# Kernel optimization log

Measured on AMD Instinct MI355X. Metric: run time of the kernel, lower is better.

Reference implementation:

```python
import jax, jax.numpy as jnp
import numpy as np

SEQ, PREV, BS, D_IN, H, D = 512, 512, 8, 1024, 16, 64


def setup_inputs() -> dict:
    key = jax.random.key(0)
    ks = jax.random.split(key, 10)
    s = 0.02
    inp = {
        "input_": jax.random.normal(ks[0], (SEQ, BS, D_IN), jnp.float32),
        "pos_embs": jax.random.normal(ks[1], (SEQ + PREV, D_IN), jnp.float32),
        "memory": jax.random.normal(ks[2], (PREV, BS, D_IN), jnp.float32),
        "u": jax.random.normal(ks[3], (H, D), jnp.float32) * s,
        "v": jax.random.normal(ks[4], (H, D), jnp.float32) * s,
        # causal mask allowing full attention to memory: triu with diagonal=1+prev
        "mask": (jnp.triu(jnp.ones((SEQ, SEQ + PREV), jnp.bool_), k=1 + PREV))[..., None],
        "W_kv": jax.random.normal(ks[5], (D_IN, 2 * H * D), jnp.float32) * s,
        "W_q": jax.random.normal(ks[6], (D_IN, H * D), jnp.float32) * s,
        "W_p": jax.random.normal(ks[7], (D_IN, H * D), jnp.float32) * s,
        "W_out": jax.random.normal(ks[8], (H * D, D_IN), jnp.float32) * s,
        "ln_gamma": jnp.ones((D_IN,), jnp.float32),
        "ln_beta": jnp.zeros((D_IN,), jnp.float32),
    }
    return inp


def _rel_shift(x):
    # x: (q, k, bs, H) -> pad one zero column, reshape-transpose trick, drop first row
    q, k, bs, h = x.shape
    zp = jnp.zeros((q, 1, bs, h), x.dtype)
    return jnp.concatenate([zp, x], axis=1).reshape(k + 1, q, bs, h)[1:].reshape(q, k, bs, h)


def reference(input_, pos_embs, memory, u, v, mask, W_kv, W_q, W_p, W_out, ln_gamma, ln_beta):
    cur_seq, bs, d_in = input_.shape
    prev_seq = memory.shape[0]
    tot = cur_seq + prev_seq
    h, d = u.shape
    scale = 1.0 / d ** 0.5

    iwm = jnp.concatenate([memory, input_], axis=0)          # (tot, bs, d_in)
    kv = jnp.einsum('jbe,ef->jbf', iwm, W_kv)                 # (tot, bs, 2*H*d)
    k_t, v_t = jnp.split(kv, 2, axis=-1)
    q_t = jnp.einsum('ibe,ef->ibf', input_, W_q)              # (cur, bs, H*d)

    q4 = q_t.reshape(cur_seq, bs, h, d)
    k4 = k_t.reshape(tot, bs, h, d)
    v4 = v_t.reshape(tot, bs, h, d)

    content_attn = jnp.einsum('ibhd,jbhd->ijbh', q4 + u, k4)  # (cur, tot, bs, H)

    p_t = (pos_embs @ W_p).reshape(tot, h, d)                 # (tot, H, d)
    position_attn = jnp.einsum('ibhd,jhd->ijbh', q4 + v, p_t)
    position_attn = _rel_shift(position_attn)

    attn = content_attn + position_attn
    attn = jnp.where(mask[..., None], -jnp.inf, attn)         # mask: (cur, tot, 1) -> (cur, tot, 1, 1)
    attn = jax.nn.softmax(attn * scale, axis=1)

    awv = jnp.einsum('ijbh,jbhd->ibhd', attn, v4).reshape(cur_seq, bs, h * d)
    out = input_ + awv @ W_out                                # residual

    mu = jnp.mean(out, axis=-1, keepdims=True)
    var = jnp.mean((out - mu) ** 2, axis=-1, keepdims=True)
    out = (out - mu) / jnp.sqrt(var + 1e-5) * ln_gamma + ln_beta
    return out
```

## Files before the change

kernel.cpp:

```cpp
#include <hip/hip_runtime.h>
#include <math.h>

#define SEQ  512
#define PREV 512
#define TOT  1024
#define BSZ  8
#define DIN  1024
#define NH   16
#define HD   64

typedef __bf16 bf16;
typedef __bf16 bf16x8 __attribute__((ext_vector_type(8)));
typedef float  f32x4  __attribute__((ext_vector_type(4)));
typedef float  f32x16 __attribute__((ext_vector_type(16)));
typedef unsigned int u32;
typedef u32 u32x2 __attribute__((ext_vector_type(2)));

__device__ __forceinline__ f32x4 MFMA16(bf16x8 a, bf16x8 b, f32x4 c) {
    return __builtin_amdgcn_mfma_f32_16x16x32_bf16(a, b, c, 0, 0, 0);
}
__device__ __forceinline__ f32x16 MFMA32(bf16x8 a, bf16x8 b, f32x16 c) {
    return __builtin_amdgcn_mfma_f32_32x32x16_bf16(a, b, c, 0, 0, 0);
}

#define GLOAD16(g, l) __builtin_amdgcn_global_load_lds( \
    (const __attribute__((address_space(1))) void*)(g), \
    (__attribute__((address_space(3))) void*)(l), 16, 0, 0)

__device__ __forceinline__ unsigned short bfbits(float x) {
    return __builtin_bit_cast(unsigned short, (bf16)x);
}
__device__ __forceinline__ float bf2f(u32 bits16) {
    return __builtin_bit_cast(float, bits16 << 16);
}

__global__ __launch_bounds__(256) void prep_all(
    const float* __restrict__ memory, const float* __restrict__ input_,
    const float* __restrict__ pos,
    const float* __restrict__ W_kv, const float* __restrict__ W_q,
    const float* __restrict__ W_p,  const float* __restrict__ W_out,
    bf16* __restrict__ iwm, bf16* __restrict__ posb,
    bf16* __restrict__ wkv, bf16* __restrict__ wq,
    bf16* __restrict__ wp,  bf16* __restrict__ wo)
{
    __shared__ float tile[32][33];
    const int bid = blockIdx.x;
    const int t = threadIdx.x;
    if (bid < 9216) {
        const float* src; bf16* dst; int e4;
        if (bid < 8192) {
            e4 = (bid * 256 + t) * 4;
            src = (e4 < 4194304) ? memory : input_ - 4194304;
            dst = iwm;
        } else {
            e4 = ((bid - 8192) * 256 + t) * 4;
            src = pos; dst = posb;
        }
        float4 x = *(const float4*)(src + e4);
        union { bf16 h[4]; ushort4 u4; } pk;
        pk.h[0] = (bf16)x.x; pk.h[1] = (bf16)x.y; pk.h[2] = (bf16)x.z; pk.h[3] = (bf16)x.w;
        *(ushort4*)(dst + e4) = pk.u4;
        return;
    }
    const int rem = bid - 9216;
    const int bx = rem % 160, by = rem / 160;
    const float* W; bf16* Wt; int N, bn;
    if (bx < 64)       { W = W_kv;  Wt = wkv; N = 2048; bn = bx * 32; }
    else if (bx < 96)  { W = W_q;   Wt = wq;  N = 1024; bn = (bx - 64) * 32; }
    else if (bx < 128) { W = W_p;   Wt = wp;  N = 1024; bn = (bx - 96) * 32; }
    else               { W = W_out; Wt = wo;  N = 1024; bn = (bx - 128) * 32; }
    const int bk = by * 32;
    const int r = t >> 3, c4 = (t & 7) * 4;
    float4 x = *(const float4*)(W + (size_t)(bk + r) * N + bn + c4);
    tile[r][c4 + 0] = x.x; tile[r][c4 + 1] = x.y;
    tile[r][c4 + 2] = x.z; tile[r][c4 + 3] = x.w;
    __syncthreads();
    union { bf16 h[4]; ushort4 u4; } pk;
#pragma unroll
    for (int i = 0; i < 4; ++i) pk.h[i] = (bf16)tile[c4 + i][r];
    *(ushort4*)(Wt + (size_t)(bn + r) * 1024 + bk + c4) = pk.u4;
}

__global__ __launch_bounds__(512, 1) void gemm_8ph(
    const bf16* __restrict__ A, const bf16* __restrict__ Bt,
    bf16* __restrict__ C, int M, int N, int K)
{
    __shared__ __align__(16) bf16 A_s[2][256 * 64];
    __shared__ __align__(16) bf16 B_s[2][256 * 64];
    const int t = threadIdx.x;
    const int w = t >> 6, lane = t & 63;
    const int li = lane & 15, hi = lane >> 4;
    const int wm = w >> 2, wn = w & 3;
    const int lin = blockIdx.y * 8 + blockIdx.x;
    const int xcd = lin & 7, idx = lin >> 3;
    const int bm = (xcd * 4 + (idx & 3)) * 256;
    const int bn = (idx >> 2) * 256;

    f32x4 acc[8][4];
#pragma unroll
    for (int m = 0; m < 8; ++m)
#pragma unroll
        for (int n = 0; n < 4; ++n) acc[m][n] = (f32x4){0.f, 0.f, 0.f, 0.f};

    auto stage_half = [&](int buf, int ks, int h) {
        const bf16* __restrict__ src = (h < 2) ? A : Bt;
        const int base = (h < 2) ? bm : bn;
        const int hh = (h & 1) * 128;
        bf16* dst = (h < 2) ? &A_s[buf][0] : &B_s[buf][0];
        const int k0 = ks << 6;
#pragma unroll
        for (int g = 0; g < 2; ++g) {
            const int row = hh + g * 64 + (t >> 3);
            const bf16* gp = src + (size_t)(base + row) * K + k0 + (((t & 7) ^ (row & 7)) * 8);
            GLOAD16(gp, dst + (size_t)(hh + g * 64 + w * 8) * 64);
        }
    };

    bf16x8 af[4], bfr[4];
    auto LDA = [&](int buf, int mh, int kk) {
#pragma unroll
        for (int m = 0; m < 4; ++m) {
            int row = wm * 128 + (mh * 4 + m) * 16 + li;
            af[m] = *(const bf16x8*)&A_s[buf][row * 64 + (((kk * 4 + hi) ^ (row & 7)) * 8)];
        }
    };
    auto LDB = [&](int buf, int kk) {
#pragma unroll
        for (int n = 0; n < 4; ++n) {
            int row = wn * 64 + n * 16 + li;
            bfr[n] = *(const bf16x8*)&B_s[buf][row * 64 + (((kk * 4 + hi) ^ (row & 7)) * 8)];
        }
    };

#define FMA_PHASE(mh)                                                    \
    asm volatile("s_waitcnt lgkmcnt(0)" ::: "memory");                   \
    __builtin_amdgcn_sched_barrier(0);                                   \
    __builtin_amdgcn_s_setprio(1);                                       \
    _Pragma("unroll")                                                    \
    for (int m = 0; m < 4; ++m)                                          \
        _Pragma("unroll")                                                \
        for (int n = 0; n < 4; ++n)                                      \
            acc[(mh) * 4 + m][n] = MFMA16(af[m], bfr[n], acc[(mh) * 4 + m][n]); \
    __builtin_amdgcn_s_setprio(0);

    stage_half(0, 0, 0); stage_half(0, 0, 1); stage_half(0, 0, 2); stage_half(0, 0, 3);

    const int nk = K >> 6;
    for (int ks = 0; ks < nk; ++ks) {
        const int cur = ks & 1, nxt = cur ^ 1;
        asm volatile("s_waitcnt vmcnt(0)" ::: "memory");
        __builtin_amdgcn_sched_barrier(0);
        __builtin_amdgcn_s_barrier();
        __builtin_amdgcn_sched_barrier(0);
        if (ks + 1 < nk) {
            stage_half(nxt, ks + 1, 0); stage_half(nxt, ks + 1, 1);
            stage_half(nxt, ks + 1, 2); stage_half(nxt, ks + 1, 3);
        }
        LDB(cur, 0); LDA(cur, 0, 0);
        FMA_PHASE(0)
        LDA(cur, 1, 0);
        FMA_PHASE(1)
        LDB(cur, 1); LDA(cur, 0, 1);
        FMA_PHASE(0)
        LDA(cur, 1, 1);
        FMA_PHASE(1)
    }

#pragma unroll
    for (int m = 0; m < 8; ++m)
#pragma unroll
        for (int n = 0; n < 4; ++n)
#pragma unroll
            for (int r = 0; r < 4; ++r) {
                int row = bm + wm * 128 + m * 16 + hi * 4 + r;
                int col = bn + wn * 64 + n * 16 + li;
                C[(size_t)row * N + col] = (bf16)acc[m][n][r];
            }
#undef FMA_PHASE
}

__global__ __launch_bounds__(256) void gemm_out(
    const bf16* __restrict__ A, const bf16* __restrict__ Bt,
    const float* __restrict__ Rres, float* __restrict__ Cf, int N, int K)
{
    __shared__ __align__(16) bf16 A_s[128 * 64];
    __shared__ __align__(16) bf16 B_s[128 * 64];
    const int t = threadIdx.x;
    const int w = t >> 6, lane = t & 63;
    const int li = lane & 15, hi = lane >> 4;
    const int wr = w >> 1, wc = w & 1;
    const int bm = blockIdx.y * 128, bn = blockIdx.x * 128;
    const int l3 = lane >> 3, l7 = lane & 7;
    const int srcoct = ((l7 ^ l3) * 8);

    f32x4 acc[4][4];
#pragma unroll
    for (int m = 0; m < 4; ++m)
#pragma unroll
        for (int n = 0; n < 4; ++n) acc[m][n] = (f32x4){0.f, 0.f, 0.f, 0.f};

    auto stage = [&](int k0) {
#pragma unroll
        for (int i = 0; i < 4; ++i) {
            int c = w * 4 + i;
            GLOAD16(A + (size_t)(bm + c * 8 + l3) * K + k0 + srcoct, &A_s[c * 512]);
            GLOAD16(Bt + (size_t)(bn + c * 8 + l3) * K + k0 + srcoct, &B_s[c * 512]);
        }
    };

    stage(0);
    const int nk = K >> 6;
    for (int ks = 0; ks < nk; ++ks) {
        __syncthreads();
#pragma unroll
        for (int kk = 0; kk < 2; ++kk) {
            bf16x8 af[4], bfr[4];
#pragma unroll
            for (int m = 0; m < 4; ++m) {
                int row = wr * 64 + m * 16 + li;
                af[m] = *(const bf16x8*)&A_s[row * 64 + ((kk * 32 + hi * 8) ^ ((row & 7) * 8))];
            }
#pragma unroll
            for (int n = 0; n < 4; ++n) {
                int row = wc * 64 + n * 16 + li;
                bfr[n] = *(const bf16x8*)&B_s[row * 64 + ((kk * 32 + hi * 8) ^ ((row & 7) * 8))];
            }
#pragma unroll
            for (int m = 0; m < 4; ++m)
#pragma unroll
                for (int n = 0; n < 4; ++n)
                    acc[m][n] = MFMA16(af[m], bfr[n], acc[m][n]);
        }
        __syncthreads();
        if (ks + 1 < nk) stage((ks + 1) << 6);
    }

#pragma unroll
    for (int m = 0; m < 4; ++m)
#pragma unroll
        for (int n = 0; n < 4; ++n)
#pragma unroll
            for (int r = 0; r < 4; ++r) {
                int row = bm + wr * 64 + m * 16 + hi * 4 + r;
                int col = bn + wc * 64 + n * 16 + li;
                size_t off = (size_t)row * N + col;
                Cf[off] = acc[m][n][r] + Rres[off];
            }
}

__global__ __launch_bounds__(256) void gemm_qp(
    const bf16* __restrict__ iwmq, const bf16* __restrict__ posb,
    const bf16* __restrict__ wq, const bf16* __restrict__ wp,
    bf16* __restrict__ qbf, bf16* __restrict__ pbf)
{
    __shared__ __align__(16) bf16 A_s[128 * 64];
    __shared__ __align__(16) bf16 B_s[128 * 64];
    const int t = threadIdx.x;
    const int w = t >> 6, lane = t & 63;
    const int li = lane & 15, hi = lane >> 4;
    const int wr = w >> 1, wc = w & 1;
    const int by = blockIdx.y;
    const bf16* A; const bf16* Bt; bf16* Cb; int bm;
    if (by < 32) { A = iwmq; Bt = wq; Cb = qbf; bm = by * 128; }
    else         { A = posb; Bt = wp; Cb = pbf; bm = (by - 32) * 128; }
    const int bn = blockIdx.x * 128;
    const int l3 = lane >> 3, l7 = lane & 7;
    const int srcoct = ((l7 ^ l3) * 8);

    f32x4 acc[4][4];
#pragma unroll
    for (int m = 0; m < 4; ++m)
#pragma unroll
        for (int n = 0; n < 4; ++n) acc[m][n] = (f32x4){0.f, 0.f, 0.f, 0.f};

    auto stage = [&](int k0) {
#pragma unroll
        for (int i = 0; i < 4; ++i) {
            int c = w * 4 + i;
            GLOAD16(A + (size_t)(bm + c * 8 + l3) * 1024 + k0 + srcoct, &A_s[c * 512]);
            GLOAD16(Bt + (size_t)(bn + c * 8 + l3) * 1024 + k0 + srcoct, &B_s[c * 512]);
        }
    };

    stage(0);
    for (int ks = 0; ks < 16; ++ks) {
        __syncthreads();
#pragma unroll
        for (int kk = 0; kk < 2; ++kk) {
            bf16x8 af[4], bfr[4];
#pragma unroll
            for (int m = 0; m < 4; ++m) {
                int row = wr * 64 + m * 16 + li;
                af[m] = *(const bf16x8*)&A_s[row * 64 + ((kk * 32 + hi * 8) ^ ((row & 7) * 8))];
            }
#pragma unroll
            for (int n = 0; n < 4; ++n) {
                int row = wc * 64 + n * 16 + li;
                bfr[n] = *(const bf16x8*)&B_s[row * 64 + ((kk * 32 + hi * 8) ^ ((row & 7) * 8))];
            }
#pragma unroll
            for (int m = 0; m < 4; ++m)
#pragma unroll
                for (int n = 0; n < 4; ++n)
                    acc[m][n] = MFMA16(af[m], bfr[n], acc[m][n]);
        }
        __syncthreads();
        if (ks + 1 < 16) stage((ks + 1) << 6);
    }

#pragma unroll
    for (int m = 0; m < 4; ++m)
#pragma unroll
        for (int n = 0; n < 4; ++n)
#pragma unroll
            for (int r = 0; r < 4; ++r) {
                int row = bm + wr * 64 + m * 16 + hi * 4 + r;
                int col = bn + wc * 64 + n * 16 + li;
                Cb[(size_t)row * 1024 + col] = (bf16)acc[m][n][r];
            }
}

__global__ __launch_bounds__(256, 2) void attn_mfma(
    const bf16* __restrict__ kv, const bf16* __restrict__ qb,
    const bf16* __restrict__ pb, const float* __restrict__ u,
    const float* __restrict__ v, bf16* __restrict__ awv)
{
    const int bi = (blockIdx.z & 1) ? (3 - blockIdx.x) : blockIdx.x;
    const int i0 = bi * 128;
    const int b  = blockIdx.y;
    const int h  = blockIdx.z;
    const int t  = threadIdx.x;
    const int w  = t >> 6;
    const int lane = t & 63;
    const int ql  = lane & 31;
    const int hi2 = lane >> 5;

    __shared__ __align__(16) bf16 K_s[64 * 64];
    __shared__ __align__(16) bf16 V_s[64][72];
    __shared__ __align__(16) bf16 P_s[256 * 64];
    __shared__ __align__(16) char SCR[4][6912];

    char* rsc = SCR[w];

    const int c8 = t & 7;
    const int rq = t >> 3;
    const int nt = 2 * bi + 10;
    const int C0 = 384 - i0;

    bf16x8 vreg[2];
#pragma unroll
    for (int p = 0; p < 2; ++p)
        vreg[p] = *(const bf16x8*)(kv + (size_t)((p * 32 + rq) * BSZ + b) * 2048 + 1024 + h * HD + c8 * 8);
#pragma unroll
    for (int p = 0; p < 2; ++p)
        GLOAD16(kv + (size_t)((p * 32 + rq) * BSZ + b) * 2048 + h * HD + ((c8 ^ (rq & 7)) * 8),
                K_s + (p * 32 + rq) * 64 + c8 * 8);
#pragma unroll
    for (int cp = 0; cp < 6; ++cp) {
        int grow = C0 + cp * 32 + rq;
        GLOAD16(pb + (size_t)grow * DIN + h * HD + ((c8 ^ (rq & 7)) * 8),
                P_s + (grow & 255) * 64 + c8 * 8);
    }

    bf16x8 qu[4], qv[4];
    {
        const size_t qoff = ((size_t)(i0 + w * 32 + ql) * BSZ + b) * DIN + h * HD;
#pragma unroll
        for (int kk = 0; kk < 4; ++kk) {
            bf16x8 q8 = *(const bf16x8*)(qb + qoff + kk * 16 + hi2 * 8);
            const float* up = u + h * HD + kk * 16 + hi2 * 8;
            const float* vp = v + h * HD + kk * 16 + hi2 * 8;
#pragma unroll
            for (int m = 0; m < 8; ++m) {
                float qf = (float)q8[m];
                qu[kk][m] = (bf16)(qf + up[m]);
                qv[kk][m] = (bf16)(qf + vp[m]);
            }
        }
    }

    float mrun = -1e30f, lrun = 0.f;
    f32x16 o[2];
    o[0] = (f32x16){}; o[1] = (f32x16){};

    const int phq = (31 - ql) & 3;
    const int sel = phq >> 1;
    const int shb = (phq & 1) * 16;

    for (int tt = 0; tt < nt; ++tt) {
        const int j0 = tt * 64;

        __builtin_amdgcn_s_barrier();
        __builtin_amdgcn_sched_barrier(0);

#pragma unroll
        for (int p = 0; p < 2; ++p) {
            int j = p * 32 + rq;
#pragma unroll
            for (int mm = 0; mm < 8; ++mm)
                V_s[c8 * 8 + mm][(j + 8 * c8) & 63] = vreg[p][mm];
        }
        asm volatile("s_waitcnt vmcnt(0) lgkmcnt(0)" ::: "memory");
        __builtin_amdgcn_sched_barrier(0);
        __builtin_amdgcn_s_barrier();
        __builtin_amdgcn_sched_barrier(0);

        f32x16 st[2];
        st[0] = (f32x16){}; st[1] = (f32x16){};
        __builtin_amdgcn_s_setprio(1);
#pragma unroll
        for (int jt = 0; jt < 2; ++jt) {
            int row = jt * 32 + ql;
#pragma unroll
            for (int kk = 0; kk < 4; ++kk) {
                bf16x8 kf = *(const bf16x8*)&K_s[row * 64 + (((kk * 2 + hi2) ^ (ql & 7)) * 8)];
                st[jt] = MFMA32(kf, qu[kk], st[jt]);
            }
        }
        const int bwg = j0 - i0 + 480 - 32 * w;
        f32x16 rp[3];
        rp[0] = (f32x16){}; rp[1] = (f32x16){}; rp[2] = (f32x16){};
#pragma unroll
        for (int Rt = 0; Rt < 3; ++Rt) {
            int ring = (bwg + Rt * 32 + ql) & 255;
#pragma unroll
            for (int kk = 0; kk < 4; ++kk) {
                bf16x8 pf = *(const bf16x8*)&P_s[ring * 64 + (((kk * 2 + hi2) ^ (ring & 7)) * 8)];
                rp[Rt] = MFMA32(pf, qv[kk], rp[Rt]);
            }
        }
        __builtin_amdgcn_s_setprio(0);

#pragma unroll
        for (int Rt = 0; Rt < 3; ++Rt)
#pragma unroll
            for (int a = 0; a < 4; ++a) {
                u32 lo = (u32)bfbits(rp[Rt][a * 4 + 0]) | ((u32)bfbits(rp[Rt][a * 4 + 1]) << 16);
                u32 hi = (u32)bfbits(rp[Rt][a * 4 + 2]) | ((u32)bfbits(rp[Rt][a * 4 + 3]) << 16);
                *(u32x2*)(rsc + ql * 216 + 64 * Rt + 16 * a + 8 * hi2) = (u32x2){lo, hi};
            }

        __builtin_amdgcn_s_barrier();
        __builtin_amdgcn_sched_barrier(0);

        if (tt + 1 < nt) {
            const int j0n = j0 + 64;
#pragma unroll
            for (int p = 0; p < 2; ++p)
                vreg[p] = *(const bf16x8*)(kv + (size_t)((j0n + p * 32 + rq) * BSZ + b) * 2048 + 1024 + h * HD + c8 * 8);
#pragma unroll
            for (int p = 0; p < 2; ++p)
                GLOAD16(kv + (size_t)((j0n + p * 32 + rq) * BSZ + b) * 2048 + h * HD + ((c8 ^ (rq & 7)) * 8),
                        K_s + (p * 32 + rq) * 64 + c8 * 8);
        }
        if (tt + 3 < nt) {
            const int Cs = C0 + (tt + 3) * 64;
#pragma unroll
            for (int p = 0; p < 2; ++p) {
                int grow = Cs + p * 32 + rq;
                GLOAD16(pb + (size_t)grow * DIN + h * HD + ((c8 ^ (rq & 7)) * 8),
                        P_s + (grow & 255) * 64 + c8 * 8);
            }
        }

        float rowmax = -1e30f;
        const int limb = i0 + 32 * w + ql + PREV - j0;
        auto assemble = [&](bool domask) {
#pragma unroll
            for (int jt = 0; jt < 2; ++jt)
#pragma unroll
                for (int a = 0; a < 4; ++a) {
                    int e = jt * 32 + 8 * a + 4 * hi2 + 31 - ql;
                    const u32x2* W = (const u32x2*)(rsc + ql * 216 + 8 * (e >> 2));
                    u32x2 A0 = W[0], A1 = W[1];
                    u32 U0 = sel ? A0[1] : A0[0];
                    u32 U1 = sel ? A1[0] : A0[1];
                    u32 U2 = sel ? A1[1] : A1[0];
                    u32 o0 = (u32)((((unsigned long long)U1 << 32) | U0) >> shb);
                    u32 o1 = (u32)((((unsigned long long)U2 << 32) | U1) >> shb);
                    float pq[4] = {bf2f(o0 & 0xffffu), bf2f(o0 >> 16),
                                   bf2f(o1 & 0xffffu), bf2f(o1 >> 16)};
#pragma unroll
                    for (int rr = 0; rr < 4; ++rr) {
                        int r = a * 4 + rr;
                        int lj = jt * 32 + 8 * a + 4 * hi2 + rr;
                        float sv = (st[jt][r] + pq[rr]) * 0.125f;
                        if (domask && lj > limb) sv = -1e30f;
                        st[jt][r] = sv;
                        rowmax = fmaxf(rowmax, sv);
                    }
                }
        };
        if (__builtin_amdgcn_readfirstlane(j0 + 63 - (i0 + 32 * w + PREV)) > 0)
            assemble(true);
        else
            assemble(false);

        {
            u32 rm = __builtin_bit_cast(u32, rowmax), rm2 = rm;
            asm("v_permlane32_swap_b32 %0, %1" : "+v"(rm), "+v"(rm2));
            rowmax = fmaxf(__builtin_bit_cast(float, rm2), __builtin_bit_cast(float, rm) * 0.f + rowmax);
            rowmax = fmaxf(rowmax, __builtin_bit_cast(float, rm2));
        }

        if (!__all(rowmax - mrun <= 8.f)) {
            float newm = fmaxf(mrun, rowmax);
            float fsc = __expf(mrun - newm);
#pragma unroll
            for (int r = 0; r < 16; ++r) {
                float fr = __shfl(fsc, (r & 3) + 8 * (r >> 2) + 4 * hi2);
                o[0][r] *= fr; o[1][r] *= fr;
            }
            lrun *= fsc;
            mrun = newm;
        }
        float rowsum = 0.f;
#pragma unroll
        for (int jt = 0; jt < 2; ++jt)
#pragma unroll
            for (int r = 0; r < 16; ++r) {
                float p = __expf(st[jt][r] - mrun);
                st[jt][r] = p;
                rowsum += p;
            }
        {
            u32 rs = __builtin_bit_cast(u32, rowsum), rs2 = rs;
            asm("v_permlane32_swap_b32 %0, %1" : "+v"(rs), "+v"(rs2));
            rowsum += __builtin_bit_cast(float, rs2);
        }
        lrun += rowsum;

        u32 pk0[2][4], pk1[2][4];
#pragma unroll
        for (int jt = 0; jt < 2; ++jt)
#pragma unroll
            for (int a = 0; a < 4; ++a) {
                pk0[jt][a] = (u32)bfbits(st[jt][a * 4 + 0]) | ((u32)bfbits(st[jt][a * 4 + 1]) << 16);
                pk1[jt][a] = (u32)bfbits(st[jt][a * 4 + 2]) | ((u32)bfbits(st[jt][a * 4 + 3]) << 16);
            }

        __builtin_amdgcn_s_setprio(1);
#pragma unroll
        for (int js = 0; js < 4; ++js) {
            const int jt = js >> 1, a0 = 2 * (js & 1), a1 = a0 + 1;
            u32 w0 = pk0[jt][a0], w2 = pk0[jt][a1];
            asm("v_permlane32_swap_b32 %0, %1" : "+v"(w0), "+v"(w2));
            u32 w1 = pk1[jt][a0], w3 = pk1[jt][a1];
            asm("v_permlane32_swap_b32 %0, %1" : "+v"(w1), "+v"(w3));
            union { u32 uw[4]; bf16x8 vv; } pa;
            pa.uw[0] = w0; pa.uw[1] = w1; pa.uw[2] = w2; pa.uw[3] = w3;
#pragma unroll
            for (int dt = 0; dt < 2; ++dt) {
                int dcol = dt * 32 + ql;
                int colb = (js * 16 + hi2 * 8 + 8 * (dcol >> 3)) & 63;
                bf16x8 vf = *(const bf16x8*)&V_s[dcol][colb];
                o[dt] = MFMA32(pa.vv, vf, o[dt]);
            }
        }
        __builtin_amdgcn_s_setprio(0);
    }

    float linv = __builtin_amdgcn_rcpf(lrun);
    float lr[16];
#pragma unroll
    for (int r = 0; r < 16; ++r) lr[r] = __shfl(linv, (r & 3) + 8 * (r >> 2) + 4 * hi2);
#pragma unroll
    for (int dt = 0; dt < 2; ++dt)
#pragma unroll
        for (int r = 0; r < 16; ++r) {
            int row = i0 + 32 * w + (r & 3) + 8 * (r >> 2) + 4 * hi2;
            awv[((size_t)row * BSZ + b) * DIN + h * HD + dt * 32 + ql] = (bf16)(o[dt][r] * lr[r]);
        }
}

__global__ __launch_bounds__(256) void ln_f32(
    float* __restrict__ out, const float* __restrict__ gamma, const float* __restrict__ beta)
{
    const int row = blockIdx.x;
    const int t = threadIdx.x;
    float4 x = *(float4*)(out + (size_t)row * DIN + t * 4);
    float s  = x.x + x.y + x.z + x.w;
    float ss = x.x * x.x + x.y * x.y + x.z * x.z + x.w * x.w;
#pragma unroll
    for (int wd = 1; wd < 64; wd <<= 1) { s += __shfl_xor(s, wd); ss += __shfl_xor(ss, wd); }
    __shared__ float sbuf[4], ssbuf[4];
    const int wave = t >> 6, lanei = t & 63;
    if (lanei == 0) { sbuf[wave] = s; ssbuf[wave] = ss; }
    __syncthreads();
    s  = sbuf[0] + sbuf[1] + sbuf[2] + sbuf[3];
    ss = ssbuf[0] + ssbuf[1] + ssbuf[2] + ssbuf[3];
    const float mu   = s * (1.f / DIN);
    const float var  = ss * (1.f / DIN) - mu * mu;
    const float rstd = rsqrtf(var + 1e-5f);
    float4 g  = *(const float4*)(gamma + t * 4);
    float4 bb = *(const float4*)(beta + t * 4);
    float4 y;
    y.x = (x.x - mu) * rstd * g.x + bb.x;
    y.y = (x.y - mu) * rstd * g.y + bb.y;
    y.z = (x.z - mu) * rstd * g.z + bb.z;
    y.w = (x.w - mu) * rstd * g.w + bb.w;
    *(float4*)(out + (size_t)row * DIN + t * 4) = y;
}

extern "C" void kernel_launch(void* const* d_in, const int* in_sizes, int n_in,
                              void* d_out, int out_size, void* d_ws, size_t ws_size,
                              hipStream_t stream)
{
    const float* input_ = (const float*)d_in[0];
    const float* pos    = (const float*)d_in[1];
    const float* memory = (const float*)d_in[2];
    const float* u      = (const float*)d_in[3];
    const float* v      = (const float*)d_in[4];
    const float* W_kv   = (const float*)d_in[6];
    const float* W_q    = (const float*)d_in[7];
    const float* W_p    = (const float*)d_in[8];
    const float* W_out  = (const float*)d_in[9];
    const float* gamma  = (const float*)d_in[10];
    const float* beta   = (const float*)d_in[11];

    bf16* iwm  = (bf16*)d_ws;
    bf16* kvb  = iwm  + (size_t)8192 * 1024;
    bf16* qbf  = kvb  + (size_t)8192 * 2048;
    bf16* pbf  = qbf  + (size_t)4096 * 1024;
    bf16* posb = pbf  + (size_t)1024 * 1024;
    bf16* wkv  = posb + (size_t)1024 * 1024;
    bf16* wq   = wkv  + (size_t)2048 * 1024;
    bf16* wp   = wq   + (size_t)1024 * 1024;
    bf16* wo   = wp   + (size_t)1024 * 1024;
    bf16* awvb = wo   + (size_t)1024 * 1024;
    float* outf = (float*)d_out;

    prep_all<<<14336, 256, 0, stream>>>(memory, input_, pos, W_kv, W_q, W_p, W_out,
                                        iwm, posb, wkv, wq, wp, wo);

    gemm_8ph<<<dim3(8, 32), 512, 0, stream>>>(iwm, wkv, kvb, 8192, 2048, 1024);
    gemm_qp<<<dim3(8, 40), 256, 0, stream>>>(iwm + (size_t)4096 * 1024, posb, wq, wp, qbf, pbf);

    attn_mfma<<<dim3(4, 8, 16), 256, 0, stream>>>(kvb, qbf, pbf, u, v, awvb);

    gemm_out<<<dim3(8, 32), 256, 0, stream>>>(awvb, wo, input_, outf, 1024, 1024);
    ln_f32<<<4096, 256, 0, stream>>>(outf, gamma, beta);
}
```

Before: 170.4 us.

## Switch KV GEMM to 32x32 MFMA with 4 waves and double-buffer output GEMM

The KV projection GEMM moves from 8 waves using 16x16x32 MFMAs to 4 waves using 32x32x16 MFMAs, each wave owning a 128x128 sub-tile. Staging and LDS reads are rewritten for the new fragment layout. The output GEMM gains double-buffered LDS with loads prefetched one step ahead, a single barrier per step, and raised wave priority around its MFMAs. A rowmax reduction in attention is also simplified. The larger MFMA shape aims for more compute per LDS read, at the cost of fewer waves to hide latency and higher register pressure.

```diff
diff --git a/kernel.cpp b/kernel.cpp
--- a/kernel.cpp
+++ b/kernel.cpp
@@ -81,7 +81,7 @@
     *(ushort4*)(Wt + (size_t)(bn + r) * 1024 + bk + c4) = pk.u4;
 }
 
-__global__ __launch_bounds__(512, 1) void gemm_8ph(
+__global__ __launch_bounds__(256, 1) void gemm_kv(
     const bf16* __restrict__ A, const bf16* __restrict__ Bt,
     bf16* __restrict__ C, int M, int N, int K)
 {
@@ -89,18 +89,20 @@
     __shared__ __align__(16) bf16 B_s[2][256 * 64];
     const int t = threadIdx.x;
     const int w = t >> 6, lane = t & 63;
-    const int li = lane & 15, hi = lane >> 4;
-    const int wm = w >> 2, wn = w & 3;
+    const int ql = lane & 31, hi2 = lane >> 5;
+    const int wm = w >> 1, wn = w & 1;
     const int lin = blockIdx.y * 8 + blockIdx.x;
     const int xcd = lin & 7, idx = lin >> 3;
     const int bm = (xcd * 4 + (idx & 3)) * 256;
     const int bn = (idx >> 2) * 256;
 
-    f32x4 acc[8][4];
-#pragma unroll
-    for (int m = 0; m < 8; ++m)
-#pragma unroll
-        for (int n = 0; n < 4; ++n) acc[m][n] = (f32x4){0.f, 0.f, 0.f, 0.f};
+    f32x16 acc[4][4];
+#pragma unroll
+    for (int mf = 0; mf < 4; ++mf)
+#pragma unroll
+        for (int nf = 0; nf < 4; ++nf) acc[mf][nf] = (f32x16){};
+
+    const int l7 = lane & 7, l3 = lane >> 3;
 
     auto stage_half = [&](int buf, int ks, int h) {
         const bf16* __restrict__ src = (h < 2) ? A : Bt;
@@ -109,39 +111,28 @@
         bf16* dst = (h < 2) ? &A_s[buf][0] : &B_s[buf][0];
         const int k0 = ks << 6;
 #pragma unroll
-        for (int g = 0; g < 2; ++g) {
-            const int row = hh + g * 64 + (t >> 3);
-            const bf16* gp = src + (size_t)(base + row) * K + k0 + (((t & 7) ^ (row & 7)) * 8);
-            GLOAD16(gp, dst + (size_t)(hh + g * 64 + w * 8) * 64);
+        for (int g = 0; g < 4; ++g) {
+            const int row = hh + g * 32 + 8 * w + l3;
+            const bf16* gp = src + (size_t)(base + row) * K + k0 + ((l7 ^ (row & 7)) * 8);
+            GLOAD16(gp, dst + (size_t)row * 64 + l7 * 8);
         }
     };
 
     bf16x8 af[4], bfr[4];
-    auto LDA = [&](int buf, int mh, int kk) {
-#pragma unroll
-        for (int m = 0; m < 4; ++m) {
-            int row = wm * 128 + (mh * 4 + m) * 16 + li;
-            af[m] = *(const bf16x8*)&A_s[buf][row * 64 + (((kk * 4 + hi) ^ (row & 7)) * 8)];
+    auto LDA = [&](int buf, int kt) {
+#pragma unroll
+        for (int mf = 0; mf < 4; ++mf) {
+            int row = wm * 128 + mf * 32 + ql;
+            af[mf] = *(const bf16x8*)&A_s[buf][(size_t)row * 64 + (((kt * 2 + hi2) ^ (row & 7)) * 8)];
         }
     };
-    auto LDB = [&](int buf, int kk) {
-#pragma unroll
-        for (int n = 0; n < 4; ++n) {
-            int row = wn * 64 + n * 16 + li;
-            bfr[n] = *(const bf16x8*)&B_s[buf][row * 64 + (((kk * 4 + hi) ^ (row & 7)) * 8)];
+    auto LDB = [&](int buf, int kt) {
+#pragma unroll
+        for (int nf = 0; nf < 4; ++nf) {
+            int row = wn * 128 + nf * 32 + ql;
+            bfr[nf] = *(const bf16x8*)&B_s[buf][(size_t)row * 64 + (((kt * 2 + hi2) ^ (row & 7)) * 8)];
         }
     };
-
-#define FMA_PHASE(mh)                                                    \
-    asm volatile("s_waitcnt lgkmcnt(0)" ::: "memory");                   \
-    __builtin_amdgcn_sched_barrier(0);                                   \
-    __builtin_amdgcn_s_setprio(1);                                       \
-    _Pragma("unroll")                                                    \
-    for (int m = 0; m < 4; ++m)                                          \
-        _Pragma("unroll")                                                \
-        for (int n = 0; n < 4; ++n)                                      \
-            acc[(mh) * 4 + m][n] = MFMA16(af[m], bfr[n], acc[(mh) * 4 + m][n]); \
-    __builtin_amdgcn_s_setprio(0);
 
     stage_half(0, 0, 0); stage_half(0, 0, 1); stage_half(0, 0, 2); stage_half(0, 0, 3);
 
@@ -156,35 +147,39 @@
             stage_half(nxt, ks + 1, 0); stage_half(nxt, ks + 1, 1);
             stage_half(nxt, ks + 1, 2); stage_half(nxt, ks + 1, 3);
         }
-        LDB(cur, 0); LDA(cur, 0, 0);
-        FMA_PHASE(0)
-        LDA(cur, 1, 0);
-        FMA_PHASE(1)
-        LDB(cur, 1); LDA(cur, 0, 1);
-        FMA_PHASE(0)
-        LDA(cur, 1, 1);
-        FMA_PHASE(1)
+#pragma unroll
+        for (int kt = 0; kt < 4; ++kt) {
+            LDA(cur, kt); LDB(cur, kt);
+            asm volatile("s_waitcnt lgkmcnt(0)" ::: "memory");
+            __builtin_amdgcn_sched_barrier(0);
+            __builtin_amdgcn_s_setprio(1);
+#pragma unroll
+            for (int mf = 0; mf < 4; ++mf)
+#pragma unroll
+                for (int nf = 0; nf < 4; ++nf)
+                    acc[mf][nf] = MFMA32(af[mf], bfr[nf], acc[mf][nf]);
+            __builtin_amdgcn_s_setprio(0);
+        }
     }
 
 #pragma unroll
-    for (int m = 0; m < 8; ++m)
-#pragma unroll
-        for (int n = 0; n < 4; ++n)
-#pragma unroll
-            for (int r = 0; r < 4; ++r) {
-                int row = bm + wm * 128 + m * 16 + hi * 4 + r;
-                int col = bn + wn * 64 + n * 16 + li;
-                C[(size_t)row * N + col] = (bf16)acc[m][n][r];
-            }
-#undef FMA_PHASE
+    for (int mf = 0; mf < 4; ++mf)
+#pragma unroll
+        for (int nf = 0; nf < 4; ++nf)
+#pragma unroll
+            for (int r = 0; r < 16; ++r) {
+                int row = bm + wm * 128 + mf * 32 + (r & 3) + 8 * (r >> 2) + 4 * hi2;
+                int col = bn + wn * 128 + nf * 32 + ql;
+                C[(size_t)row * N + col] = (bf16)acc[mf][nf][r];
+            }
 }
 
 __global__ __launch_bounds__(256) void gemm_out(
     const bf16* __restrict__ A, const bf16* __restrict__ Bt,
     const float* __restrict__ Rres, float* __restrict__ Cf, int N, int K)
 {
-    __shared__ __align__(16) bf16 A_s[128 * 64];
-    __shared__ __align__(16) bf16 B_s[128 * 64];
+    __shared__ __align__(16) bf16 A_s[2][128 * 64];
+    __shared__ __align__(16) bf16 B_s[2][128 * 64];
     const int t = threadIdx.x;
     const int w = t >> 6, lane = t & 63;
     const int li = lane & 15, hi = lane >> 4;
@@ -199,40 +194,47 @@
 #pragma unroll
         for (int n = 0; n < 4; ++n) acc[m][n] = (f32x4){0.f, 0.f, 0.f, 0.f};
 
-    auto stage = [&](int k0) {
+    auto stage = [&](int buf, int k0) {
 #pragma unroll
         for (int i = 0; i < 4; ++i) {
             int c = w * 4 + i;
-            GLOAD16(A + (size_t)(bm + c * 8 + l3) * K + k0 + srcoct, &A_s[c * 512]);
-            GLOAD16(Bt + (size_t)(bn + c * 8 + l3) * K + k0 + srcoct, &B_s[c * 512]);
+            GLOAD16(A + (size_t)(bm + c * 8 + l3) * K + k0 + srcoct, &A_s[buf][c * 512]);
+            GLOAD16(Bt + (size_t)(bn + c * 8 + l3) * K + k0 + srcoct, &B_s[buf][c * 512]);
         }
     };
 
-    stage(0);
+    stage(0, 0);
     const int nk = K >> 6;
     for (int ks = 0; ks < nk; ++ks) {
-        __syncthreads();
+        const int cur = ks & 1, nxt = cur ^ 1;
+        asm volatile("s_waitcnt vmcnt(0)" ::: "memory");
+        __builtin_amdgcn_sched_barrier(0);
+        __builtin_amdgcn_s_barrier();
+        __builtin_amdgcn_sched_barrier(0);
+        if (ks + 1 < nk) stage(nxt, (ks + 1) << 6);
 #pragma unroll
         for (int kk = 0; kk < 2; ++kk) {
             bf16x8 af[4], bfr[4];
 #pragma unroll
             for (int m = 0; m < 4; ++m) {
                 int row = wr * 64 + m * 16 + li;
-                af[m] = *(const bf16x8*)&A_s[row * 64 + ((kk * 32 + hi * 8) ^ ((row & 7) * 8))];
+                af[m] = *(const bf16x8*)&A_s[cur][row * 64 + ((kk * 32 + hi * 8) ^ ((row & 7) * 8))];
             }
 #pragma unroll
             for (int n = 0; n < 4; ++n) {
                 int row = wc * 64 + n * 16 + li;
-                bfr[n] = *(const bf16x8*)&B_s[row * 64 + ((kk * 32 + hi * 8) ^ ((row & 7) * 8))];
-            }
+                bfr[n] = *(const bf16x8*)&B_s[cur][row * 64 + ((kk * 32 + hi * 8) ^ ((row & 7) * 8))];
+            }
+            asm volatile("s_waitcnt lgkmcnt(0)" ::: "memory");
+            __builtin_amdgcn_sched_barrier(0);
+            __builtin_amdgcn_s_setprio(1);
 #pragma unroll
             for (int m = 0; m < 4; ++m)
 #pragma unroll
                 for (int n = 0; n < 4; ++n)
                     acc[m][n] = MFMA16(af[m], bfr[n], acc[m][n]);
-        }
-        __syncthreads();
-        if (ks + 1 < nk) stage((ks + 1) << 6);
+            __builtin_amdgcn_s_setprio(0);
+        }
     }
 
 #pragma unroll
@@ -499,7 +501,7 @@
         {
             u32 rm = __builtin_bit_cast(u32, rowmax), rm2 = rm;
             asm("v_permlane32_swap_b32 %0, %1" : "+v"(rm), "+v"(rm2));
-            rowmax = fmaxf(__builtin_bit_cast(float, rm2), __builtin_bit_cast(float, rm) * 0.f + rowmax);
+            rowmax = fmaxf(rowmax, __builtin_bit_cast(float, rm));
             rowmax = fmaxf(rowmax, __builtin_bit_cast(float, rm2));
         }
 
@@ -633,7 +635,7 @@
     prep_all<<<14336, 256, 0, stream>>>(memory, input_, pos, W_kv, W_q, W_p, W_out,
                                         iwm, posb, wkv, wq, wp, wo);
 
-    gemm_8ph<<<dim3(8, 32), 512, 0, stream>>>(iwm, wkv, kvb, 8192, 2048, 1024);
+    gemm_kv<<<dim3(8, 32), 256, 0, stream>>>(iwm, wkv, kvb, 8192, 2048, 1024);
     gemm_qp<<<dim3(8, 40), 256, 0, stream>>>(iwm + (size_t)4096 * 1024, posb, wq, wp, qbf, pbf);
 
     attn_mfma<<<dim3(4, 8, 16), 256, 0, stream>>>(kvb, qbf, pbf, u, v, awvb);
```

Measured after the change: 174.0 us. 1.02x slower.

## Fuse fp32-to-bf16 activation conversion into GEMMs, double-buffer gemm_out, use exp2 softmax

Applied to the files above, without the earlier changes.

Stops pre-converting memory, input and pos_embs to bf16 in a separate pass. The KV and Q/P GEMMs now load the fp32 rows directly, convert them in registers and write swizzled bf16 into LDS, which removes a full write and re-read of the activations. gemm_out gets double-buffered LDS with explicit waitcnt and priority hints. The attention softmax folds log2(e) into the scale and uses a raw v_exp_f32, with the rescale threshold adjusted to match. The cost is more VGPR pressure and extra conversion work inside the GEMM loops, and the fp32 A loads are now regular register loads rather than direct-to-LDS.

```diff
diff --git a/kernel.cpp b/kernel.cpp
--- a/kernel.cpp
+++ b/kernel.cpp
@@ -33,43 +33,27 @@
 __device__ __forceinline__ float bf2f(u32 bits16) {
     return __builtin_bit_cast(float, bits16 << 16);
 }
-
-__global__ __launch_bounds__(256) void prep_all(
-    const float* __restrict__ memory, const float* __restrict__ input_,
-    const float* __restrict__ pos,
+__device__ __forceinline__ float exp2_raw(float x) {
+    float r;
+    asm("v_exp_f32 %0, %1" : "=v"(r) : "v"(x));
+    return r;
+}
+
+__global__ __launch_bounds__(256) void prep_w(
     const float* __restrict__ W_kv, const float* __restrict__ W_q,
     const float* __restrict__ W_p,  const float* __restrict__ W_out,
-    bf16* __restrict__ iwm, bf16* __restrict__ posb,
     bf16* __restrict__ wkv, bf16* __restrict__ wq,
     bf16* __restrict__ wp,  bf16* __restrict__ wo)
 {
     __shared__ float tile[32][33];
-    const int bid = blockIdx.x;
+    const int bx = blockIdx.x;
     const int t = threadIdx.x;
-    if (bid < 9216) {
-        const float* src; bf16* dst; int e4;
-        if (bid < 8192) {
-            e4 = (bid * 256 + t) * 4;
-            src = (e4 < 4194304) ? memory : input_ - 4194304;
-            dst = iwm;
-        } else {
-            e4 = ((bid - 8192) * 256 + t) * 4;
-            src = pos; dst = posb;
-        }
-        float4 x = *(const float4*)(src + e4);
-        union { bf16 h[4]; ushort4 u4; } pk;
-        pk.h[0] = (bf16)x.x; pk.h[1] = (bf16)x.y; pk.h[2] = (bf16)x.z; pk.h[3] = (bf16)x.w;
-        *(ushort4*)(dst + e4) = pk.u4;
-        return;
-    }
-    const int rem = bid - 9216;
-    const int bx = rem % 160, by = rem / 160;
     const float* W; bf16* Wt; int N, bn;
     if (bx < 64)       { W = W_kv;  Wt = wkv; N = 2048; bn = bx * 32; }
     else if (bx < 96)  { W = W_q;   Wt = wq;  N = 1024; bn = (bx - 64) * 32; }
     else if (bx < 128) { W = W_p;   Wt = wp;  N = 1024; bn = (bx - 96) * 32; }
     else               { W = W_out; Wt = wo;  N = 1024; bn = (bx - 128) * 32; }
-    const int bk = by * 32;
+    const int bk = blockIdx.y * 32;
     const int r = t >> 3, c4 = (t & 7) * 4;
     float4 x = *(const float4*)(W + (size_t)(bk + r) * N + bn + c4);
     tile[r][c4 + 0] = x.x; tile[r][c4 + 1] = x.y;
@@ -81,9 +65,9 @@
     *(ushort4*)(Wt + (size_t)(bn + r) * 1024 + bk + c4) = pk.u4;
 }
 
-__global__ __launch_bounds__(512, 1) void gemm_8ph(
-    const bf16* __restrict__ A, const bf16* __restrict__ Bt,
-    bf16* __restrict__ C, int M, int N, int K)
+__global__ __launch_bounds__(512, 1) void gemm_kv(
+    const float* __restrict__ memory, const float* __restrict__ input_,
+    const bf16* __restrict__ wkv, bf16* __restrict__ kvb)
 {
     __shared__ __align__(16) bf16 A_s[2][256 * 64];
     __shared__ __align__(16) bf16 B_s[2][256 * 64];
@@ -95,6 +79,9 @@
     const int xcd = lin & 7, idx = lin >> 3;
     const int bm = (xcd * 4 + (idx & 3)) * 256;
     const int bn = (idx >> 2) * 256;
+    const float* __restrict__ srcA = (bm < 4096) ? memory + (size_t)bm * 1024
+                                                 : input_ + (size_t)(bm - 4096) * 1024;
+    const int arow = t >> 1, aoct = (t & 1) * 4;
 
     f32x4 acc[8][4];
 #pragma unroll
@@ -102,17 +89,33 @@
 #pragma unroll
         for (int n = 0; n < 4; ++n) acc[m][n] = (f32x4){0.f, 0.f, 0.f, 0.f};
 
-    auto stage_half = [&](int buf, int ks, int h) {
-        const bf16* __restrict__ src = (h < 2) ? A : Bt;
-        const int base = (h < 2) ? bm : bn;
-        const int hh = (h & 1) * 128;
-        bf16* dst = (h < 2) ? &A_s[buf][0] : &B_s[buf][0];
+    float4 areg[4][2];
+    auto issueA = [&](int ks) {
+        const float* rp = srcA + (size_t)arow * 1024 + ks * 64;
+#pragma unroll
+        for (int c = 0; c < 4; ++c) {
+            areg[c][0] = *(const float4*)(rp + (aoct + c) * 8);
+            areg[c][1] = *(const float4*)(rp + (aoct + c) * 8 + 4);
+        }
+    };
+    auto writeA = [&](int buf) {
+#pragma unroll
+        for (int c = 0; c < 4; ++c) {
+            union { bf16 h[8]; bf16x8 v; } pk;
+            pk.h[0] = (bf16)areg[c][0].x; pk.h[1] = (bf16)areg[c][0].y;
+            pk.h[2] = (bf16)areg[c][0].z; pk.h[3] = (bf16)areg[c][0].w;
+            pk.h[4] = (bf16)areg[c][1].x; pk.h[5] = (bf16)areg[c][1].y;
+            pk.h[6] = (bf16)areg[c][1].z; pk.h[7] = (bf16)areg[c][1].w;
+            *(bf16x8*)&A_s[buf][arow * 64 + (((aoct + c) ^ (arow & 7)) * 8)] = pk.v;
+        }
+    };
+    auto stageB = [&](int buf, int ks) {
         const int k0 = ks << 6;
 #pragma unroll
-        for (int g = 0; g < 2; ++g) {
-            const int row = hh + g * 64 + (t >> 3);
-            const bf16* gp = src + (size_t)(base + row) * K + k0 + (((t & 7) ^ (row & 7)) * 8);
-            GLOAD16(gp, dst + (size_t)(hh + g * 64 + w * 8) * 64);
+        for (int g = 0; g < 4; ++g) {
+            const int row = g * 64 + (t >> 3);
+            GLOAD16(wkv + (size_t)(bn + row) * 1024 + k0 + (((t & 7) ^ (row & 7)) * 8),
+                    &B_s[buf][(size_t)row * 64 + (t & 7) * 8]);
         }
     };
 
@@ -143,19 +146,18 @@
             acc[(mh) * 4 + m][n] = MFMA16(af[m], bfr[n], acc[(mh) * 4 + m][n]); \
     __builtin_amdgcn_s_setprio(0);
 
-    stage_half(0, 0, 0); stage_half(0, 0, 1); stage_half(0, 0, 2); stage_half(0, 0, 3);
-
-    const int nk = K >> 6;
+    issueA(0);
+    stageB(0, 0);
+    writeA(0);
+    asm volatile("s_waitcnt vmcnt(0) lgkmcnt(0)" ::: "memory");
+    __builtin_amdgcn_sched_barrier(0);
+    __builtin_amdgcn_s_barrier();
+    __builtin_amdgcn_sched_barrier(0);
+
+    const int nk = 16;
     for (int ks = 0; ks < nk; ++ks) {
         const int cur = ks & 1, nxt = cur ^ 1;
-        asm volatile("s_waitcnt vmcnt(0)" ::: "memory");
-        __builtin_amdgcn_sched_barrier(0);
-        __builtin_amdgcn_s_barrier();
-        __builtin_amdgcn_sched_barrier(0);
-        if (ks + 1 < nk) {
-            stage_half(nxt, ks + 1, 0); stage_half(nxt, ks + 1, 1);
-            stage_half(nxt, ks + 1, 2); stage_half(nxt, ks + 1, 3);
-        }
+        if (ks + 1 < nk) { issueA(ks + 1); stageB(nxt, ks + 1); }
         LDB(cur, 0); LDA(cur, 0, 0);
         FMA_PHASE(0)
         LDA(cur, 1, 0);
@@ -164,7 +166,17 @@
         FMA_PHASE(0)
         LDA(cur, 1, 1);
         FMA_PHASE(1)
+        if (ks + 1 < nk) {
+            asm volatile("s_waitcnt vmcnt(4)" ::: "memory");
+            __builtin_amdgcn_sched_barrier(0);
+            writeA(nxt);
+            asm volatile("s_waitcnt vmcnt(0) lgkmcnt(0)" ::: "memory");
+            __builtin_amdgcn_sched_barrier(0);
+        }
+        __builtin_amdgcn_s_barrier();
+        __builtin_amdgcn_sched_barrier(0);
     }
+#undef FMA_PHASE
 
 #pragma unroll
     for (int m = 0; m < 8; ++m)
@@ -174,82 +186,12 @@
             for (int r = 0; r < 4; ++r) {
                 int row = bm + wm * 128 + m * 16 + hi * 4 + r;
                 int col = bn + wn * 64 + n * 16 + li;
-                C[(size_t)row * N + col] = (bf16)acc[m][n][r];
-            }
-#undef FMA_PHASE
-}
-
-__global__ __launch_bounds__(256) void gemm_out(
-    const bf16* __restrict__ A, const bf16* __restrict__ Bt,
-    const float* __restrict__ Rres, float* __restrict__ Cf, int N, int K)
-{
-    __shared__ __align__(16) bf16 A_s[128 * 64];
-    __shared__ __align__(16) bf16 B_s[128 * 64];
-    const int t = threadIdx.x;
-    const int w = t >> 6, lane = t & 63;
-    const int li = lane & 15, hi = lane >> 4;
-    const int wr = w >> 1, wc = w & 1;
-    const int bm = blockIdx.y * 128, bn = blockIdx.x * 128;
-    const int l3 = lane >> 3, l7 = lane & 7;
-    const int srcoct = ((l7 ^ l3) * 8);
-
-    f32x4 acc[4][4];
-#pragma unroll
-    for (int m = 0; m < 4; ++m)
-#pragma unroll
-        for (int n = 0; n < 4; ++n) acc[m][n] = (f32x4){0.f, 0.f, 0.f, 0.f};
-
-    auto stage = [&](int k0) {
-#pragma unroll
-        for (int i = 0; i < 4; ++i) {
-            int c = w * 4 + i;
-            GLOAD16(A + (size_t)(bm + c * 8 + l3) * K + k0 + srcoct, &A_s[c * 512]);
-            GLOAD16(Bt + (size_t)(bn + c * 8 + l3) * K + k0 + srcoct, &B_s[c * 512]);
-        }
-    };
-
-    stage(0);
-    const int nk = K >> 6;
-    for (int ks = 0; ks < nk; ++ks) {
-        __syncthreads();
-#pragma unroll
-        for (int kk = 0; kk < 2; ++kk) {
-            bf16x8 af[4], bfr[4];
-#pragma unroll
-            for (int m = 0; m < 4; ++m) {
-                int row = wr * 64 + m * 16 + li;
-                af[m] = *(const bf16x8*)&A_s[row * 64 + ((kk * 32 + hi * 8) ^ ((row & 7) * 8))];
-            }
-#pragma unroll
-            for (int n = 0; n < 4; ++n) {
-                int row = wc * 64 + n * 16 + li;
-                bfr[n] = *(const bf16x8*)&B_s[row * 64 + ((kk * 32 + hi * 8) ^ ((row & 7) * 8))];
-            }
-#pragma unroll
-            for (int m = 0; m < 4; ++m)
-#pragma unroll
-                for (int n = 0; n < 4; ++n)
-                    acc[m][n] = MFMA16(af[m], bfr[n], acc[m][n]);
-        }
-        __syncthreads();
-        if (ks + 1 < nk) stage((ks + 1) << 6);
-    }
-
-#pragma unroll
-    for (int m = 0; m < 4; ++m)
-#pragma unroll
-        for (int n = 0; n < 4; ++n)
-#pragma unroll
-            for (int r = 0; r < 4; ++r) {
-                int row = bm + wr * 64 + m * 16 + hi * 4 + r;
-                int col = bn + wc * 64 + n * 16 + li;
-                size_t off = (size_t)row * N + col;
-                Cf[off] = acc[m][n][r] + Rres[off];
+                kvb[(size_t)row * 2048 + col] = (bf16)acc[m][n][r];
             }
 }
 
 __global__ __launch_bounds__(256) void gemm_qp(
-    const bf16* __restrict__ iwmq, const bf16* __restrict__ posb,
+    const float* __restrict__ input_, const float* __restrict__ pos,
     const bf16* __restrict__ wq, const bf16* __restrict__ wp,
     bf16* __restrict__ qbf, bf16* __restrict__ pbf)
 {
@@ -260,12 +202,13 @@
     const int li = lane & 15, hi = lane >> 4;
     const int wr = w >> 1, wc = w & 1;
     const int by = blockIdx.y;
-    const bf16* A; const bf16* Bt; bf16* Cb; int bm;
-    if (by < 32) { A = iwmq; Bt = wq; Cb = qbf; bm = by * 128; }
-    else         { A = posb; Bt = wp; Cb = pbf; bm = (by - 32) * 128; }
+    const float* srcA; const bf16* Bt; bf16* Cb; int bm;
+    if (by < 32) { srcA = input_; Bt = wq; Cb = qbf; bm = by * 128; }
+    else         { srcA = pos;    Bt = wp; Cb = pbf; bm = (by - 32) * 128; }
     const int bn = blockIdx.x * 128;
     const int l3 = lane >> 3, l7 = lane & 7;
     const int srcoct = ((l7 ^ l3) * 8);
+    const int arow = t >> 1, aoct = (t & 1) * 4;
 
     f32x4 acc[4][4];
 #pragma unroll
@@ -273,18 +216,40 @@
 #pragma unroll
         for (int n = 0; n < 4; ++n) acc[m][n] = (f32x4){0.f, 0.f, 0.f, 0.f};
 
-    auto stage = [&](int k0) {
+    float4 areg[4][2];
+    auto issueA = [&](int ks) {
+        const float* rp = srcA + (size_t)(bm + arow) * 1024 + ks * 64;
+#pragma unroll
+        for (int c = 0; c < 4; ++c) {
+            areg[c][0] = *(const float4*)(rp + (aoct + c) * 8);
+            areg[c][1] = *(const float4*)(rp + (aoct + c) * 8 + 4);
+        }
+    };
+    auto writeA = [&]() {
+#pragma unroll
+        for (int c = 0; c < 4; ++c) {
+            union { bf16 h[8]; bf16x8 v; } pk;
+            pk.h[0] = (bf16)areg[c][0].x; pk.h[1] = (bf16)areg[c][0].y;
+            pk.h[2] = (bf16)areg[c][0].z; pk.h[3] = (bf16)areg[c][0].w;
+            pk.h[4] = (bf16)areg[c][1].x; pk.h[5] = (bf16)areg[c][1].y;
+            pk.h[6] = (bf16)areg[c][1].z; pk.h[7] = (bf16)areg[c][1].w;
+            *(bf16x8*)&A_s[arow * 64 + (((aoct + c) ^ (arow & 7)) * 8)] = pk.v;
+        }
+    };
+    auto stageB = [&](int k0) {
 #pragma unroll
         for (int i = 0; i < 4; ++i) {
             int c = w * 4 + i;
-            GLOAD16(A + (size_t)(bm + c * 8 + l3) * 1024 + k0 + srcoct, &A_s[c * 512]);
             GLOAD16(Bt + (size_t)(bn + c * 8 + l3) * 1024 + k0 + srcoct, &B_s[c * 512]);
         }
     };
 
-    stage(0);
+    issueA(0);
+    writeA();
+    stageB(0);
     for (int ks = 0; ks < 16; ++ks) {
         __syncthreads();
+        if (ks + 1 < 16) issueA(ks + 1);
 #pragma unroll
         for (int kk = 0; kk < 2; ++kk) {
             bf16x8 af[4], bfr[4];
@@ -305,7 +270,7 @@
                     acc[m][n] = MFMA16(af[m], bfr[n], acc[m][n]);
         }
         __syncthreads();
-        if (ks + 1 < 16) stage((ks + 1) << 6);
+        if (ks + 1 < 16) { writeA(); stageB((ks + 1) << 6); }
     }
 
 #pragma unroll
@@ -317,6 +282,82 @@
                 int row = bm + wr * 64 + m * 16 + hi * 4 + r;
                 int col = bn + wc * 64 + n * 16 + li;
                 Cb[(size_t)row * 1024 + col] = (bf16)acc[m][n][r];
+            }
+}
+
+__global__ __launch_bounds__(256) void gemm_out(
+    const bf16* __restrict__ A, const bf16* __restrict__ Bt,
+    const float* __restrict__ Rres, float* __restrict__ Cf, int N, int K)
+{
+    __shared__ __align__(16) bf16 A_s[2][128 * 64];
+    __shared__ __align__(16) bf16 B_s[2][128 * 64];
+    const int t = threadIdx.x;
+    const int w = t >> 6, lane = t & 63;
+    const int li = lane & 15, hi = lane >> 4;
+    const int wr = w >> 1, wc = w & 1;
+    const int bm = blockIdx.y * 128, bn = blockIdx.x * 128;
+    const int l3 = lane >> 3, l7 = lane & 7;
+    const int srcoct = ((l7 ^ l3) * 8);
+
+    f32x4 acc[4][4];
+#pragma unroll
+    for (int m = 0; m < 4; ++m)
+#pragma unroll
+        for (int n = 0; n < 4; ++n) acc[m][n] = (f32x4){0.f, 0.f, 0.f, 0.f};
+
+    auto stage = [&](int buf, int k0) {
+#pragma unroll
+        for (int i = 0; i < 4; ++i) {
+            int c = w * 4 + i;
+            GLOAD16(A + (size_t)(bm + c * 8 + l3) * K + k0 + srcoct, &A_s[buf][c * 512]);
+            GLOAD16(Bt + (size_t)(bn + c * 8 + l3) * K + k0 + srcoct, &B_s[buf][c * 512]);
+        }
+    };
+
+    stage(0, 0);
+    const int nk = K >> 6;
+    for (int ks = 0; ks < nk; ++ks) {
+        const int cur = ks & 1, nxt = cur ^ 1;
+        asm volatile("s_waitcnt vmcnt(0)" ::: "memory");
+        __builtin_amdgcn_sched_barrier(0);
+        __builtin_amdgcn_s_barrier();
+        __builtin_amdgcn_sched_barrier(0);
+        if (ks + 1 < nk) stage(nxt, (ks + 1) << 6);
+#pragma unroll
+        for (int kk = 0; kk < 2; ++kk) {
+            bf16x8 af[4], bfr[4];
+#pragma unroll
+            for (int m = 0; m < 4; ++m) {
+                int row = wr * 64 + m * 16 + li;
+                af[m] = *(const bf16x8*)&A_s[cur][row * 64 + ((kk * 32 + hi * 8) ^ ((row & 7) * 8))];
+            }
+#pragma unroll
+            for (int n = 0; n < 4; ++n) {
+                int row = wc * 64 + n * 16 + li;
+                bfr[n] = *(const bf16x8*)&B_s[cur][row * 64 + ((kk * 32 + hi * 8) ^ ((row & 7) * 8))];
+            }
+            asm volatile("s_waitcnt lgkmcnt(0)" ::: "memory");
+            __builtin_amdgcn_sched_barrier(0);
+            __builtin_amdgcn_s_setprio(1);
+#pragma unroll
+            for (int m = 0; m < 4; ++m)
+#pragma unroll
+                for (int n = 0; n < 4; ++n)
+                    acc[m][n] = MFMA16(af[m], bfr[n], acc[m][n]);
+            __builtin_amdgcn_s_setprio(0);
+        }
+    }
+
+#pragma unroll
+    for (int m = 0; m < 4; ++m)
+#pragma unroll
+        for (int n = 0; n < 4; ++n)
+#pragma unroll
+            for (int r = 0; r < 4; ++r) {
+                int row = bm + wr * 64 + m * 16 + hi * 4 + r;
+                int col = bn + wc * 64 + n * 16 + li;
+                size_t off = (size_t)row * N + col;
+                Cf[off] = acc[m][n][r] + Rres[off];
             }
 }
 
@@ -346,6 +387,7 @@
     const int rq = t >> 3;
     const int nt = 2 * bi + 10;
     const int C0 = 384 - i0;
+    const float SCL2 = 0.125f * 1.44269504088896f;
 
     bf16x8 vreg[2];
 #pragma unroll
@@ -484,7 +526,7 @@
                     for (int rr = 0; rr < 4; ++rr) {
                         int r = a * 4 + rr;
                         int lj = jt * 32 + 8 * a + 4 * hi2 + rr;
-                        float sv = (st[jt][r] + pq[rr]) * 0.125f;
+                        float sv = (st[jt][r] + pq[rr]) * SCL2;
                         if (domask && lj > limb) sv = -1e30f;
                         st[jt][r] = sv;
                         rowmax = fmaxf(rowmax, sv);
@@ -499,13 +541,13 @@
         {
             u32 rm = __builtin_bit_cast(u32, rowmax), rm2 = rm;
             asm("v_permlane32_swap_b32 %0, %1" : "+v"(rm), "+v"(rm2));
-            rowmax = fmaxf(__builtin_bit_cast(float, rm2), __builtin_bit_cast(float, rm) * 0.f + rowmax);
+            rowmax = fmaxf(rowmax, __builtin_bit_cast(float, rm));
             rowmax = fmaxf(rowmax, __builtin_bit_cast(float, rm2));
         }
 
-        if (!__all(rowmax - mrun <= 8.f)) {
+        if (!__all(rowmax - mrun <= 11.54f)) {
             float newm = fmaxf(mrun, rowmax);
-            float fsc = __expf(mrun - newm);
+            float fsc = exp2_raw(mrun - newm);
 #pragma unroll
             for (int r = 0; r < 16; ++r) {
                 float fr = __shfl(fsc, (r & 3) + 8 * (r >> 2) + 4 * hi2);
@@ -519,7 +561,7 @@
         for (int jt = 0; jt < 2; ++jt)
 #pragma unroll
             for (int r = 0; r < 16; ++r) {
-                float p = __expf(st[jt][r] - mrun);
+                float p = exp2_raw(st[jt][r] - mrun);
                 st[jt][r] = p;
                 rowsum += p;
             }
@@ -618,23 +660,20 @@
     const float* gamma  = (const float*)d_in[10];
     const float* beta   = (const float*)d_in[11];
 
-    bf16* iwm  = (bf16*)d_ws;
-    bf16* kvb  = iwm  + (size_t)8192 * 1024;
+    bf16* kvb  = (bf16*)d_ws;
     bf16* qbf  = kvb  + (size_t)8192 * 2048;
     bf16* pbf  = qbf  + (size_t)4096 * 1024;
-    bf16* posb = pbf  + (size_t)1024 * 1024;
-    bf16* wkv  = posb + (size_t)1024 * 1024;
+    bf16* wkv  = pbf  + (size_t)1024 * 1024;
     bf16* wq   = wkv  + (size_t)2048 * 1024;
     bf16* wp   = wq   + (size_t)1024 * 1024;
     bf16* wo   = wp   + (size_t)1024 * 1024;
     bf16* awvb = wo   + (size_t)1024 * 1024;
     float* outf = (float*)d_out;
 
-    prep_all<<<14336, 256, 0, stream>>>(memory, input_, pos, W_kv, W_q, W_p, W_out,
-                                        iwm, posb, wkv, wq, wp, wo);
-
-    gemm_8ph<<<dim3(8, 32), 512, 0, stream>>>(iwm, wkv, kvb, 8192, 2048, 1024);
-    gemm_qp<<<dim3(8, 40), 256, 0, stream>>>(iwm + (size_t)4096 * 1024, posb, wq, wp, qbf, pbf);
+    prep_w<<<dim3(160, 32), 256, 0, stream>>>(W_kv, W_q, W_p, W_out, wkv, wq, wp, wo);
+
+    gemm_kv<<<dim3(8, 32), 512, 0, stream>>>(memory, input_, wkv, kvb);
+    gemm_qp<<<dim3(8, 40), 256, 0, stream>>>(input_, pos, wq, wp, qbf, pbf);
 
     attn_mfma<<<dim3(4, 8, 16), 256, 0, stream>>>(kvb, qbf, pbf, u, v, awvb);
 
```

Result: slower. 216.2 us (+26.9%).
